# Performance work log

Measured on AMD Instinct MI355X. Metric: run time of the kernel, lower is better.

Reference implementation:

```python
import jax, jax.numpy as jnp
import numpy as np

K = 9          # 3x3 deformable kernel positions
EPS = 1e-5     # BatchNorm eps


def conv3x3(x, w, stride=1):
    # x: [B,C,H,W], w: [O,I,3,3], padding=1
    return jax.lax.conv_general_dilated(
        x, w, (stride, stride), ((1, 1), (1, 1)),
        dimension_numbers=('NCHW', 'OIHW', 'NCHW'))


def _bilinear_sample(img, py, px):
    # img: [C,H,W]; py,px: [K,Ho,Wo] float sample coords (zero outside).
    H, W = img.shape[1], img.shape[2]
    y0 = jnp.floor(py)
    x0 = jnp.floor(px)

    def corner(yc, xc):
        w = (1.0 - jnp.abs(py - yc)) * (1.0 - jnp.abs(px - xc))
        valid = (yc >= 0) & (yc <= H - 1) & (xc >= 0) & (xc <= W - 1)
        yi = jnp.clip(yc, 0, H - 1).astype(jnp.int32)
        xi = jnp.clip(xc, 0, W - 1).astype(jnp.int32)
        v = img[:, yi, xi]                      # [C,K,Ho,Wo]
        return v * (w * valid)[None]

    return (corner(y0, x0) + corner(y0, x0 + 1) +
            corner(y0 + 1, x0) + corner(y0 + 1, x0 + 1))


def deform_conv2d(x, offset, mask, w, stride=1, pad=1):
    # x: [B,Cin,H,W]; offset: [B,2K,Ho,Wo] (y,x interleaved per tap);
    # mask: [B,K,Ho,Wo]; w: [Cout,Cin,3,3]. torchvision DCNv2 semantics.
    B, Cin = x.shape[0], x.shape[1]
    Ho, Wo = offset.shape[2], offset.shape[3]
    Cout = w.shape[0]
    kh, kw = jnp.meshgrid(jnp.arange(3), jnp.arange(3), indexing='ij')
    kh = kh.reshape(K).astype(x.dtype)
    kw = kw.reshape(K).astype(x.dtype)
    base_y = (jnp.arange(Ho) * stride - pad).astype(x.dtype)
    base_x = (jnp.arange(Wo) * stride - pad).astype(x.dtype)
    off = offset.reshape(B, K, 2, Ho, Wo)
    py = base_y[None, None, :, None] + kh[None, :, None, None] + off[:, :, 0]
    px = base_x[None, None, None, :] + kw[None, :, None, None] + off[:, :, 1]
    g = jax.vmap(_bilinear_sample)(x, py, px)     # [B,Cin,K,Ho,Wo]
    g = g * mask[:, None]
    return jnp.einsum('bikhw,oik->bohw', g, w.reshape(Cout, Cin, K))


def batchnorm(x, gamma, beta, mean, var):
    # eval-mode BN over channel dim of [B,C,H,W]
    inv = jax.lax.rsqrt(var + EPS) * gamma
    return x * inv[None, :, None, None] + (beta - mean * inv)[None, :, None, None]


def setup_inputs() -> dict:
    key = jax.random.key(0)
    ks = jax.random.split(key, 20)
    B, Cin, H, W = 16, 64, 64, 64
    C1, C2, NC = 128, 128, 1000
    inp = {
        'x': jax.random.normal(ks[0], (B, Cin, H, W), jnp.float32),
        'conv1_w': jax.random.normal(ks[1], (C1, Cin, 3, 3), jnp.float32) * 0.05,
        'off1_w': jax.random.normal(ks[2], (2 * K, Cin, 3, 3), jnp.float32) * 0.02,
        'mod1_w': jax.random.normal(ks[3], (K, Cin, 3, 3), jnp.float32) * 0.05,
        'bn1_g': jax.random.uniform(ks[4], (C1,), jnp.float32, 0.5, 1.5),
        'bn1_b': jax.random.normal(ks[5], (C1,), jnp.float32) * 0.1,
        'bn1_m': jax.random.normal(ks[6], (C1,), jnp.float32) * 0.1,
        'bn1_v': jax.random.uniform(ks[7], (C1,), jnp.float32, 0.5, 1.5),
        'conv2_w': jax.random.normal(ks[8], (C2, C1, 3, 3), jnp.float32) * 0.05,
        'off2_w': jax.random.normal(ks[9], (2 * K, C1, 3, 3), jnp.float32) * 0.02,
        'mod2_w': jax.random.normal(ks[10], (K, C1, 3, 3), jnp.float32) * 0.05,
        'bn2_g': jax.random.uniform(ks[11], (C2,), jnp.float32, 0.5, 1.5),
        'bn2_b': jax.random.normal(ks[12], (C2,), jnp.float32) * 0.1,
        'bn2_m': jax.random.normal(ks[13], (C2,), jnp.float32) * 0.1,
        'bn2_v': jax.random.uniform(ks[14], (C2,), jnp.float32, 0.5, 1.5),
        'fc_w': jax.random.normal(ks[15], (NC, C2), jnp.float32) * 0.05,
        'fc_b': jnp.zeros((NC,), jnp.float32),
    }
    return inp


def reference(x, conv1_w, off1_w, mod1_w, bn1_g, bn1_b, bn1_m, bn1_v,
              conv2_w, off2_w, mod2_w, bn2_g, bn2_b, bn2_m, bn2_v,
              fc_w, fc_b):
    stride = 1
    # stage 1: deformable conv (offset + sigmoid modulation) + BN + ReLU
    off = conv3x3(x, off1_w, stride)
    mask = jax.nn.sigmoid(conv3x3(x, mod1_w, stride))
    out = deform_conv2d(x, off, mask, conv1_w, stride=stride, pad=1)
    out = jax.nn.relu(batchnorm(out, bn1_g, bn1_b, bn1_m, bn1_v))
    # stage 2: deformable conv + BN (no ReLU before GAP, as in source)
    off = conv3x3(out, off2_w, stride)
    mask = jax.nn.sigmoid(conv3x3(out, mod2_w, stride))
    out = deform_conv2d(out, off, mask, conv2_w, stride=stride, pad=1)
    out = batchnorm(out, bn2_g, bn2_b, bn2_m, bn2_v)
    # global average pool + fc
    out = out.mean(axis=(2, 3))                 # [B, C2]
    return out @ fc_w.T + fc_b
```

## Files before the change

kernel.cpp:

```cpp
#include <hip/hip_runtime.h>

#define TPB 256
typedef unsigned short us;
typedef __attribute__((ext_vector_type(8))) _Float16 f16x8;
typedef __attribute__((ext_vector_type(2))) _Float16 f16x2;
typedef __attribute__((ext_vector_type(4))) float f32x4;

__device__ inline us f2h(float f){ union{ _Float16 h; us u; } x; x.h = (_Float16)f; return x.u; }
__device__ inline f16x2 u2h2(unsigned u){ union{ unsigned v; f16x2 h; } x; x.v = u; return x.h; }
#define MFMA16(a,b,c) __builtin_amdgcn_mfma_f32_16x16x32_f16((a),(b),(c),0,0,0)
#define PERM_LO 0x01000504u
#define PERM_HI 0x03020706u
__device__ inline int swz(int row, int q){ return q ^ ((row ^ (row >> 2)) & 3); }

__global__ __launch_bounds__(256) void k_transpose_x(const float* __restrict__ x,
                                                     us* __restrict__ xT){
  __shared__ float tile[64][65];
  const int y = blockIdx.x, b = blockIdx.y;
  for (int i = threadIdx.x; i < 4096; i += TPB){
    const int c = i >> 6, xx = i & 63;
    tile[c][xx] = x[b*262144 + c*4096 + y*64 + xx];
  }
  __syncthreads();
  for (int i = threadIdx.x; i < 4096; i += TPB){
    const int xx = i >> 6, c = i & 63;
    xT[(size_t)(b*4096 + y*64 + xx)*64 + c] = f2h(tile[c][xx]);
  }
}

__global__ __launch_bounds__(256) void k_prep(
    const float* __restrict__ cw1, const float* __restrict__ ow1, const float* __restrict__ mw1,
    const float* __restrict__ cw2, const float* __restrict__ ow2, const float* __restrict__ mw2,
    us* __restrict__ d1, us* __restrict__ d2, us* __restrict__ a1, us* __restrict__ a2){
  const int e = blockIdx.x*TPB + threadIdx.x;
  if (e < 73728){
    int k = e/8192, r = e%8192, kb = r/4096, r2 = r%4096;
    int n0 = r2>>9, q = r2&511, l = q>>3, j = q&7;
    int co = n0*16 + (l&15), c = kb*32 + (l>>4)*8 + j;
    d1[e] = f2h(cw1[(co*64 + c)*9 + k]);
  }
  if (e < 147456){
    int k = e/16384, r = e%16384, kb = r/4096, r2 = r%4096;
    int n0 = r2>>9, q = r2&511, l = q>>3, j = q&7;
    int co = n0*16 + (l&15), c = kb*32 + (l>>4)*8 + j;
    d2[e] = f2h(cw2[(co*128 + c)*9 + k]);
  }
  if (e < 18432){
    int k = e/2048, r = e%2048, kb = r/1024, r2 = r%1024;
    int n0 = r2>>9, q = r2&511, l = q>>3, j = q&7;
    int co = n0*16 + (l&15), c = kb*32 + (l>>4)*8 + j;
    float w = (co < 18) ? ow1[(co*64 + c)*9 + k] : (co < 27 ? mw1[((co-18)*64 + c)*9 + k] : 0.f);
    a1[e] = f2h(w);
  }
  if (e < 36864){
    int k = e/4096, r = e%4096, kb = r/1024, r2 = r%1024;
    int n0 = r2>>9, q = r2&511, l = q>>3, j = q&7;
    int co = n0*16 + (l&15), c = kb*32 + (l>>4)*8 + j;
    float w = (co < 18) ? ow2[(co*128 + c)*9 + k] : (co < 27 ? mw2[((co-18)*128 + c)*9 + k] : 0.f);
    a2[e] = f2h(w);
  }
}

template<int CIN, int STAGE>
__global__ __launch_bounds__(256, 4) void k_fused(
    const us* __restrict__ inT,
    const us* __restrict__ wb_aux, const us* __restrict__ wb_def,
    const float* __restrict__ bn_g, const float* __restrict__ bn_b,
    const float* __restrict__ bn_m, const float* __restrict__ bn_v,
    us* __restrict__ outT, float* __restrict__ partial){
  constexpr int KB   = CIN/32;
  constexpr int NC   = 9*KB;
  constexpr int WE_A = 2*KB*512;
  constexpr int WE_D = 8*KB*512;

  __shared__ __align__(16) us pool[6336];
  __shared__ uint2 otab[576];
  __shared__ uint2 wtab[576];
  __shared__ float extra[256];

  const int id  = blockIdx.x;
  const int nid = (id & 7)*128 + (id >> 3);
  const int b = nid >> 6, ho = nid & 63;
  const int tid = threadIdx.x;
  const us* __restrict__ inb = inT + (size_t)b*4096*CIN;

  if (STAGE == 1 && tid < 128){
    float inv = rsqrtf(bn_v[tid] + 1e-5f)*bn_g[tid];
    extra[tid] = inv; extra[128 + tid] = bn_b[tid] - bn_m[tid]*inv;
  }

  const int lane = tid & 63, lr = lane & 15, lg = lane >> 4;
  const int wv = tid >> 6;

  f32x4 aacc[2];
  aacc[0] = (f32x4){0.f,0.f,0.f,0.f}; aacc[1] = (f32x4){0.f,0.f,0.f,0.f};
  for (int kb = 0; kb < KB; ++kb){
    if (kb) __syncthreads();
    for (int s = tid; s < 792; s += 256){
      const int slot = s >> 2, cq = s & 3;
      const int r = slot/66, p = slot - r*66;
      const int y = ho - 1 + r, x = p - 1;
      uint4 q = make_uint4(0u,0u,0u,0u);
      if (y >= 0 && y < 64 && x >= 0 && x < 64)
        q = *(const uint4*)(inb + (size_t)(y*64 + x)*CIN + kb*32 + cq*8);
      *(uint4*)(pool + slot*32 + swz(slot, cq)*8) = q;
    }
    __syncthreads();
    #pragma unroll
    for (int k = 0; k < 9; ++k){
      const int kh = k/3, kw = k - kh*3;
      const int slot = kh*66 + wv*16 + lr + kw;
      f16x8 a = *(const f16x8*)(pool + slot*32 + swz(slot, lg)*8);
      #pragma unroll
      for (int n = 0; n < 2; ++n){
        f16x8 bf = *(const f16x8*)(wb_aux + (size_t)k*WE_A + (size_t)(kb*2 + n)*512 + lane*8);
        aacc[n] = MFMA16(a, bf, aacc[n]);
      }
    }
  }
  __syncthreads();

  float* am = (float*)pool;
  #pragma unroll
  for (int n = 0; n < 2; ++n){
    const int co = n*16 + lr;
    if (co < 27){
      #pragma unroll
      for (int i = 0; i < 4; ++i) am[co*66 + wv*16 + lg*4 + i] = aacc[n][i];
    }
  }
  __syncthreads();

  for (int it = 0; it < 3; ++it){
    const int sid = it*256 + tid;
    if (sid < 576){
      const int k = sid >> 6, px = sid & 63;
      const int kh = k/3, kw = k - kh*3;
      float oy = am[(2*k)*66 + px];
      float ox = am[(2*k+1)*66 + px];
      float mv = 1.f/(1.f + expf(-am[(18+k)*66 + px]));
      float py  = (float)(ho - 1 + kh) + oy;
      float pxx = (float)(px - 1 + kw) + ox;
      float fyf = floorf(py), fxf = floorf(pxx);
      int y0 = (int)fyf, x0 = (int)fxf;
      float dy = py - fyf, dx = pxx - fxf;
      bool vy0 = (y0 >= 0) && (y0 < 64), vy1 = (y0 >= -1) && (y0 < 63);
      bool vx0 = (x0 >= 0) && (x0 < 64), vx1 = (x0 >= -1) && (x0 < 63);
      int y0c = min(max(y0,0),63), y1c = min(max(y0+1,0),63);
      int x0c = min(max(x0,0),63), x1c = min(max(x0+1,0),63);
      otab[sid] = make_uint2((unsigned)(y0c*64 + x0c) | ((unsigned)(y0c*64 + x1c) << 16),
                             (unsigned)(y1c*64 + x0c) | ((unsigned)(y1c*64 + x1c) << 16));
      float w00 = (1.f-dy)*(1.f-dx)*mv*((vy0 && vx0) ? 1.f : 0.f);
      float w01 = (1.f-dy)*dx     *mv*((vy0 && vx1) ? 1.f : 0.f);
      float w10 = dy*(1.f-dx)     *mv*((vy1 && vx0) ? 1.f : 0.f);
      float w11 = dy*dx           *mv*((vy1 && vx1) ? 1.f : 0.f);
      wtab[sid] = make_uint2((unsigned)f2h(w00) | ((unsigned)f2h(w01) << 16),
                             (unsigned)f2h(w10) | ((unsigned)f2h(w11) << 16));
    }
  }
  __syncthreads();

  f32x4 acc[4][2];
  #pragma unroll
  for (int m = 0; m < 4; ++m){ acc[m][0] = (f32x4){0.f,0.f,0.f,0.f}; acc[m][1] = (f32x4){0.f,0.f,0.f,0.f}; }

  auto stage_def = [&](int i, us* dst){
    const int k = i/KB, kb = i - (i/KB)*KB;
    const int px = tid >> 2, cq = tid & 3;
    const uint2 o = otab[k*64 + px];
    const uint2 wp = wtab[k*64 + px];
    const f16x2 wAB = u2h2(wp.x), wCD = u2h2(wp.y);
    const int c0 = kb*32 + cq*8;
    const uint4 A = *(const uint4*)(inb + (size_t)(o.x & 0xffffu)*CIN + c0);
    const uint4 B = *(const uint4*)(inb + (size_t)(o.x >> 16)    *CIN + c0);
    const uint4 C = *(const uint4*)(inb + (size_t)(o.y & 0xffffu)*CIN + c0);
    const uint4 D = *(const uint4*)(inb + (size_t)(o.y >> 16)    *CIN + c0);
    const unsigned* Au = (const unsigned*)&A;
    const unsigned* Bu = (const unsigned*)&B;
    const unsigned* Cu = (const unsigned*)&C;
    const unsigned* Du = (const unsigned*)&D;
    uint4 r;
    unsigned* ru = (unsigned*)&r;
    #pragma unroll
    for (int jj = 0; jj < 4; ++jj){
      float vL = __builtin_amdgcn_fdot2(wAB, u2h2(__builtin_amdgcn_perm(Au[jj], Bu[jj], PERM_LO)), 0.f, false);
      vL = __builtin_amdgcn_fdot2(wCD, u2h2(__builtin_amdgcn_perm(Cu[jj], Du[jj], PERM_LO)), vL, false);
      float vH = __builtin_amdgcn_fdot2(wAB, u2h2(__builtin_amdgcn_perm(Au[jj], Bu[jj], PERM_HI)), 0.f, false);
      vH = __builtin_amdgcn_fdot2(wCD, u2h2(__builtin_amdgcn_perm(Cu[jj], Du[jj], PERM_HI)), vH, false);
      ru[jj] = (unsigned)f2h(vL) | ((unsigned)f2h(vH) << 16);
    }
    *(uint4*)(dst + px*32 + swz(px, cq)*8) = r;
  };
  auto mfma_def = [&](int i, const us* src){
    const int k = i/KB, kb = i - (i/KB)*KB;
    f16x8 a[4];
    #pragma unroll
    for (int mt = 0; mt < 4; ++mt){
      const int row = mt*16 + lr;
      a[mt] = *(const f16x8*)(src + row*32 + swz(row, lg)*8);
    }
    #pragma unroll
    for (int nt = 0; nt < 2; ++nt){
      f16x8 bf = *(const f16x8*)(wb_def + (size_t)k*WE_D + (size_t)(kb*8 + wv*2 + nt)*512 + lane*8);
      #pragma unroll
      for (int mt = 0; mt < 4; ++mt)
        acc[mt][nt] = MFMA16(a[mt], bf, acc[mt][nt]);
    }
  };

  us* g0 = pool;
  us* g1 = pool + 2048;
  stage_def(0, g0);
  __syncthreads();
  for (int i = 0; i < NC; ++i){
    us* cur = (i & 1) ? g1 : g0;
    us* nxt = (i & 1) ? g0 : g1;
    if (i + 1 < NC) stage_def(i+1, nxt);
    mfma_def(i, cur);
    __syncthreads();
  }

  if (STAGE == 1){
    const size_t rowbase = (size_t)(b*4096 + ho*64)*128;
    #pragma unroll
    for (int mt = 0; mt < 4; ++mt){
      const int pxl = mt*16 + lg*4;
      #pragma unroll
      for (int nt = 0; nt < 2; ++nt){
        const int co = (wv*2 + nt)*16 + lr;
        const float inv = extra[co], bia = extra[128 + co];
        #pragma unroll
        for (int i = 0; i < 4; ++i){
          float v = acc[mt][nt][i]*inv + bia;
          outT[rowbase + (size_t)(pxl + i)*128 + co] = f2h(fmaxf(v, 0.f));
        }
      }
    }
  } else {
    #pragma unroll
    for (int nt = 0; nt < 2; ++nt){
      float s = 0.f;
      #pragma unroll
      for (int mt = 0; mt < 4; ++mt)
        s += acc[mt][nt][0] + acc[mt][nt][1] + acc[mt][nt][2] + acc[mt][nt][3];
      s += __shfl_xor(s, 16);
      s += __shfl_xor(s, 32);
      if (lane < 16) extra[(wv*2 + nt)*16 + lane] = s;
    }
    __syncthreads();
    if (tid < 128) partial[(size_t)(b*64 + ho)*128 + tid] = extra[tid];
  }
}

__global__ __launch_bounds__(256) void k_pool(
    const float* __restrict__ partial,
    const float* __restrict__ g2, const float* __restrict__ b2,
    const float* __restrict__ m2, const float* __restrict__ v2,
    float* __restrict__ pooled){
  const int t = blockIdx.x*TPB + threadIdx.x;
  if (t >= 2048) return;
  const int b = t >> 7, c = t & 127;
  float s = 0.f;
  for (int h = 0; h < 64; ++h) s += partial[(b*64 + h)*128 + c];
  const float inv = rsqrtf(v2[c] + 1e-5f)*g2[c];
  pooled[t] = s*(1.f/4096.f)*inv + (b2[c] - m2[c]*inv);
}

__global__ __launch_bounds__(256) void k_fc(
    const float* __restrict__ pooled, const float* __restrict__ fcw,
    const float* __restrict__ fcb, float* __restrict__ outp){
  const int t = blockIdx.x*TPB + threadIdx.x;
  if (t >= 16000) return;
  const int b = t/1000, n = t - b*1000;
  const float* p = pooled + b*128;
  const float* w = fcw + n*128;
  float s = fcb[n];
  #pragma unroll
  for (int c = 0; c < 128; c += 4){
    const float4 pv = *(const float4*)(p + c);
    const float4 wv = *(const float4*)(w + c);
    s = fmaf(pv.x, wv.x, s); s = fmaf(pv.y, wv.y, s);
    s = fmaf(pv.z, wv.z, s); s = fmaf(pv.w, wv.w, s);
  }
  outp[t] = s;
}

extern "C" void kernel_launch(void* const* d_in, const int* in_sizes, int n_in,
                              void* d_out, int out_size, void* d_ws, size_t ws_size,
                              hipStream_t stream){
  const float* x      = (const float*)d_in[0];
  const float* conv1w = (const float*)d_in[1];
  const float* off1w  = (const float*)d_in[2];
  const float* mod1w  = (const float*)d_in[3];
  const float* bn1g   = (const float*)d_in[4];
  const float* bn1b   = (const float*)d_in[5];
  const float* bn1m   = (const float*)d_in[6];
  const float* bn1v   = (const float*)d_in[7];
  const float* conv2w = (const float*)d_in[8];
  const float* off2w  = (const float*)d_in[9];
  const float* mod2w  = (const float*)d_in[10];
  const float* bn2g   = (const float*)d_in[11];
  const float* bn2b   = (const float*)d_in[12];
  const float* bn2m   = (const float*)d_in[13];
  const float* bn2v   = (const float*)d_in[14];
  const float* fcw    = (const float*)d_in[15];
  const float* fcb    = (const float*)d_in[16];

  char* w = (char*)d_ws;
  us*    xT      = (us*)(w);
  us*    out1T   = (us*)(w + 8388608);
  float* partial = (float*)(w + 25165824);
  float* pooled  = (float*)(w + 25690112);
  us*    wb_d1   = (us*)(w + 25698304);
  us*    wb_d2   = (us*)(w + 25845760);
  us*    wb_a1   = (us*)(w + 26140672);
  us*    wb_a2   = (us*)(w + 26177536);

  k_transpose_x<<<dim3(64,16), TPB, 0, stream>>>(x, xT);
  k_prep<<<576, TPB, 0, stream>>>(conv1w, off1w, mod1w, conv2w, off2w, mod2w,
                                  wb_d1, wb_d2, wb_a1, wb_a2);

  k_fused<64,1><<<1024, TPB, 0, stream>>>(
      xT, wb_a1, wb_d1, bn1g, bn1b, bn1m, bn1v, out1T, nullptr);
  k_fused<128,2><<<1024, TPB, 0, stream>>>(
      out1T, wb_a2, wb_d2, nullptr, nullptr, nullptr, nullptr, nullptr, partial);

  k_pool<<<8, TPB, 0, stream>>>(partial, bn2g, bn2b, bn2m, bn2v, pooled);
  k_fc<<<63, TPB, 0, stream>>>(pooled, fcw, fcb, (float*)d_out);
}
```

Measured before the change: 112.5 us.

## Use 512-thread blocks with 64-channel K-chunks and packed f16 bilinear blend

Doubles the fused deformable-conv block to 8 waves. Each wave now owns one 16-channel output tile instead of two, and each pipeline step stages 64 input channels instead of 32, which halves the number of barrier-separated steps. The bilinear blend switches from perm+fdot2 to packed f16 vector multiply-adds, and the LDS swizzle becomes a simple XOR over 8 chunks. In exchange, shared memory per block roughly doubles and per-wave MFMA work halves. Interpolation now accumulates in f16 rather than f32, which may reduce accuracy.

```diff
diff --git a/kernel.cpp b/kernel.cpp
--- a/kernel.cpp
+++ b/kernel.cpp
@@ -9,9 +9,6 @@
 __device__ inline us f2h(float f){ union{ _Float16 h; us u; } x; x.h = (_Float16)f; return x.u; }
 __device__ inline f16x2 u2h2(unsigned u){ union{ unsigned v; f16x2 h; } x; x.v = u; return x.h; }
 #define MFMA16(a,b,c) __builtin_amdgcn_mfma_f32_16x16x32_f16((a),(b),(c),0,0,0)
-#define PERM_LO 0x01000504u
-#define PERM_HI 0x03020706u
-__device__ inline int swz(int row, int q){ return q ^ ((row ^ (row >> 2)) & 3); }
 
 __global__ __launch_bounds__(256) void k_transpose_x(const float* __restrict__ x,
                                                      us* __restrict__ xT){
@@ -62,18 +59,18 @@
 }
 
 template<int CIN, int STAGE>
-__global__ __launch_bounds__(256, 4) void k_fused(
+__global__ __launch_bounds__(512, 6) void k_fused(
     const us* __restrict__ inT,
     const us* __restrict__ wb_aux, const us* __restrict__ wb_def,
     const float* __restrict__ bn_g, const float* __restrict__ bn_b,
     const float* __restrict__ bn_m, const float* __restrict__ bn_v,
     us* __restrict__ outT, float* __restrict__ partial){
-  constexpr int KB   = CIN/32;
-  constexpr int NC   = 9*KB;
-  constexpr int WE_A = 2*KB*512;
-  constexpr int WE_D = 8*KB*512;
-
-  __shared__ __align__(16) us pool[6336];
+  constexpr int KB2  = CIN/64;
+  constexpr int NC   = 9*KB2;
+  constexpr int WE_A = 2*(CIN/32)*512;
+  constexpr int WE_D = 8*(CIN/32)*512;
+
+  __shared__ __align__(16) us pool[12672];
   __shared__ uint2 otab[576];
   __shared__ uint2 wtab[576];
   __shared__ float extra[256];
@@ -92,124 +89,115 @@
   const int lane = tid & 63, lr = lane & 15, lg = lane >> 4;
   const int wv = tid >> 6;
 
-  f32x4 aacc[2];
-  aacc[0] = (f32x4){0.f,0.f,0.f,0.f}; aacc[1] = (f32x4){0.f,0.f,0.f,0.f};
-  for (int kb = 0; kb < KB; ++kb){
-    if (kb) __syncthreads();
-    for (int s = tid; s < 792; s += 256){
-      const int slot = s >> 2, cq = s & 3;
+  const int mh = wv & 3, nh = wv >> 2;
+  f32x4 aacc = (f32x4){0.f,0.f,0.f,0.f};
+  for (int kb2 = 0; kb2 < KB2; ++kb2){
+    if (kb2) __syncthreads();
+    for (int s = tid; s < 1584; s += 512){
+      const int slot = s >> 3, cq = s & 7;
       const int r = slot/66, p = slot - r*66;
       const int y = ho - 1 + r, x = p - 1;
       uint4 q = make_uint4(0u,0u,0u,0u);
       if (y >= 0 && y < 64 && x >= 0 && x < 64)
-        q = *(const uint4*)(inb + (size_t)(y*64 + x)*CIN + kb*32 + cq*8);
-      *(uint4*)(pool + slot*32 + swz(slot, cq)*8) = q;
+        q = *(const uint4*)(inb + (size_t)(y*64 + x)*CIN + kb2*64 + cq*8);
+      *(uint4*)(pool + slot*64 + ((cq ^ (slot & 7))*8)) = q;
     }
     __syncthreads();
     #pragma unroll
     for (int k = 0; k < 9; ++k){
       const int kh = k/3, kw = k - kh*3;
-      const int slot = kh*66 + wv*16 + lr + kw;
-      f16x8 a = *(const f16x8*)(pool + slot*32 + swz(slot, lg)*8);
+      const int slot = kh*66 + mh*16 + lr + kw;
       #pragma unroll
-      for (int n = 0; n < 2; ++n){
-        f16x8 bf = *(const f16x8*)(wb_aux + (size_t)k*WE_A + (size_t)(kb*2 + n)*512 + lane*8);
-        aacc[n] = MFMA16(a, bf, aacc[n]);
+      for (int kbl = 0; kbl < 2; ++kbl){
+        f16x8 a = *(const f16x8*)(pool + slot*64 + (((kbl*4 + lg) ^ (slot & 7))*8));
+        f16x8 bf = *(const f16x8*)(wb_aux + (size_t)k*WE_A + (size_t)((kb2*2 + kbl)*2 + nh)*512 + lane*8);
+        aacc = MFMA16(a, bf, aacc);
       }
     }
   }
   __syncthreads();
 
   float* am = (float*)pool;
-  #pragma unroll
-  for (int n = 0; n < 2; ++n){
-    const int co = n*16 + lr;
+  {
+    const int co = nh*16 + lr;
     if (co < 27){
       #pragma unroll
-      for (int i = 0; i < 4; ++i) am[co*66 + wv*16 + lg*4 + i] = aacc[n][i];
-    }
-  }
-  __syncthreads();
-
-  for (int it = 0; it < 3; ++it){
-    const int sid = it*256 + tid;
-    if (sid < 576){
-      const int k = sid >> 6, px = sid & 63;
-      const int kh = k/3, kw = k - kh*3;
-      float oy = am[(2*k)*66 + px];
-      float ox = am[(2*k+1)*66 + px];
-      float mv = 1.f/(1.f + expf(-am[(18+k)*66 + px]));
-      float py  = (float)(ho - 1 + kh) + oy;
-      float pxx = (float)(px - 1 + kw) + ox;
-      float fyf = floorf(py), fxf = floorf(pxx);
-      int y0 = (int)fyf, x0 = (int)fxf;
-      float dy = py - fyf, dx = pxx - fxf;
-      bool vy0 = (y0 >= 0) && (y0 < 64), vy1 = (y0 >= -1) && (y0 < 63);
-      bool vx0 = (x0 >= 0) && (x0 < 64), vx1 = (x0 >= -1) && (x0 < 63);
-      int y0c = min(max(y0,0),63), y1c = min(max(y0+1,0),63);
-      int x0c = min(max(x0,0),63), x1c = min(max(x0+1,0),63);
-      otab[sid] = make_uint2((unsigned)(y0c*64 + x0c) | ((unsigned)(y0c*64 + x1c) << 16),
-                             (unsigned)(y1c*64 + x0c) | ((unsigned)(y1c*64 + x1c) << 16));
-      float w00 = (1.f-dy)*(1.f-dx)*mv*((vy0 && vx0) ? 1.f : 0.f);
-      float w01 = (1.f-dy)*dx     *mv*((vy0 && vx1) ? 1.f : 0.f);
-      float w10 = dy*(1.f-dx)     *mv*((vy1 && vx0) ? 1.f : 0.f);
-      float w11 = dy*dx           *mv*((vy1 && vx1) ? 1.f : 0.f);
-      wtab[sid] = make_uint2((unsigned)f2h(w00) | ((unsigned)f2h(w01) << 16),
-                             (unsigned)f2h(w10) | ((unsigned)f2h(w11) << 16));
-    }
-  }
-  __syncthreads();
-
-  f32x4 acc[4][2];
+      for (int i = 0; i < 4; ++i) am[co*66 + mh*16 + lg*4 + i] = aacc[i];
+    }
+  }
+  __syncthreads();
+
+  for (int sid = tid; sid < 576; sid += 512){
+    const int k = sid >> 6, px = sid & 63;
+    const int kh = k/3, kw = k - kh*3;
+    float oy = am[(2*k)*66 + px];
+    float ox = am[(2*k+1)*66 + px];
+    float mv = 1.f/(1.f + expf(-am[(18+k)*66 + px]));
+    float py  = (float)(ho - 1 + kh) + oy;
+    float pxx = (float)(px - 1 + kw) + ox;
+    float fyf = floorf(py), fxf = floorf(pxx);
+    int y0 = (int)fyf, x0 = (int)fxf;
+    float dy = py - fyf, dx = pxx - fxf;
+    bool vy0 = (y0 >= 0) && (y0 < 64), vy1 = (y0 >= -1) && (y0 < 63);
+    bool vx0 = (x0 >= 0) && (x0 < 64), vx1 = (x0 >= -1) && (x0 < 63);
+    int y0c = min(max(y0,0),63), y1c = min(max(y0+1,0),63);
+    int x0c = min(max(x0,0),63), x1c = min(max(x0+1,0),63);
+    otab[sid] = make_uint2((unsigned)(y0c*64 + x0c) | ((unsigned)(y0c*64 + x1c) << 16),
+                           (unsigned)(y1c*64 + x0c) | ((unsigned)(y1c*64 + x1c) << 16));
+    float w00 = (1.f-dy)*(1.f-dx)*mv*((vy0 && vx0) ? 1.f : 0.f);
+    float w01 = (1.f-dy)*dx     *mv*((vy0 && vx1) ? 1.f : 0.f);
+    float w10 = dy*(1.f-dx)     *mv*((vy1 && vx0) ? 1.f : 0.f);
+    float w11 = dy*dx           *mv*((vy1 && vx1) ? 1.f : 0.f);
+    wtab[sid] = make_uint2((unsigned)f2h(w00) | ((unsigned)f2h(w01) << 16),
+                           (unsigned)f2h(w10) | ((unsigned)f2h(w11) << 16));
+  }
+  __syncthreads();
+
+  f32x4 acc[4];
   #pragma unroll
-  for (int m = 0; m < 4; ++m){ acc[m][0] = (f32x4){0.f,0.f,0.f,0.f}; acc[m][1] = (f32x4){0.f,0.f,0.f,0.f}; }
+  for (int m = 0; m < 4; ++m) acc[m] = (f32x4){0.f,0.f,0.f,0.f};
 
   auto stage_def = [&](int i, us* dst){
-    const int k = i/KB, kb = i - (i/KB)*KB;
-    const int px = tid >> 2, cq = tid & 3;
+    const int k = i/KB2, kb2 = i - (i/KB2)*KB2;
+    const int px = tid >> 3, cq = tid & 7;
     const uint2 o = otab[k*64 + px];
     const uint2 wp = wtab[k*64 + px];
     const f16x2 wAB = u2h2(wp.x), wCD = u2h2(wp.y);
-    const int c0 = kb*32 + cq*8;
-    const uint4 A = *(const uint4*)(inb + (size_t)(o.x & 0xffffu)*CIN + c0);
-    const uint4 B = *(const uint4*)(inb + (size_t)(o.x >> 16)    *CIN + c0);
-    const uint4 C = *(const uint4*)(inb + (size_t)(o.y & 0xffffu)*CIN + c0);
-    const uint4 D = *(const uint4*)(inb + (size_t)(o.y >> 16)    *CIN + c0);
-    const unsigned* Au = (const unsigned*)&A;
-    const unsigned* Bu = (const unsigned*)&B;
-    const unsigned* Cu = (const unsigned*)&C;
-    const unsigned* Du = (const unsigned*)&D;
-    uint4 r;
-    unsigned* ru = (unsigned*)&r;
-    #pragma unroll
-    for (int jj = 0; jj < 4; ++jj){
-      float vL = __builtin_amdgcn_fdot2(wAB, u2h2(__builtin_amdgcn_perm(Au[jj], Bu[jj], PERM_LO)), 0.f, false);
-      vL = __builtin_amdgcn_fdot2(wCD, u2h2(__builtin_amdgcn_perm(Cu[jj], Du[jj], PERM_LO)), vL, false);
-      float vH = __builtin_amdgcn_fdot2(wAB, u2h2(__builtin_amdgcn_perm(Au[jj], Bu[jj], PERM_HI)), 0.f, false);
-      vH = __builtin_amdgcn_fdot2(wCD, u2h2(__builtin_amdgcn_perm(Cu[jj], Du[jj], PERM_HI)), vH, false);
-      ru[jj] = (unsigned)f2h(vL) | ((unsigned)f2h(vH) << 16);
-    }
-    *(uint4*)(dst + px*32 + swz(px, cq)*8) = r;
+    const _Float16 wA = wAB[0], wB = wAB[1], wC = wCD[0], wD = wCD[1];
+    const f16x8 va = (f16x8){wA,wA,wA,wA,wA,wA,wA,wA};
+    const f16x8 vb = (f16x8){wB,wB,wB,wB,wB,wB,wB,wB};
+    const f16x8 vc = (f16x8){wC,wC,wC,wC,wC,wC,wC,wC};
+    const f16x8 vd = (f16x8){wD,wD,wD,wD,wD,wD,wD,wD};
+    const int c0 = kb2*64 + cq*8;
+    f16x8 r;
+    {
+      const f16x8 A = *(const f16x8*)(inb + (size_t)(o.x & 0xffffu)*CIN + c0);
+      const f16x8 B = *(const f16x8*)(inb + (size_t)(o.x >> 16)    *CIN + c0);
+      r = A*va + B*vb;
+    }
+    {
+      const f16x8 C = *(const f16x8*)(inb + (size_t)(o.y & 0xffffu)*CIN + c0);
+      const f16x8 D = *(const f16x8*)(inb + (size_t)(o.y >> 16)    *CIN + c0);
+      r = r + C*vc + D*vd;
+    }
+    *(f16x8*)(dst + px*64 + ((cq ^ (px & 7))*8)) = r;
   };
   auto mfma_def = [&](int i, const us* src){
-    const int k = i/KB, kb = i - (i/KB)*KB;
-    f16x8 a[4];
+    const int k = i/KB2, kb2 = i - (i/KB2)*KB2;
     #pragma unroll
-    for (int mt = 0; mt < 4; ++mt){
-      const int row = mt*16 + lr;
-      a[mt] = *(const f16x8*)(src + row*32 + swz(row, lg)*8);
-    }
-    #pragma unroll
-    for (int nt = 0; nt < 2; ++nt){
-      f16x8 bf = *(const f16x8*)(wb_def + (size_t)k*WE_D + (size_t)(kb*8 + wv*2 + nt)*512 + lane*8);
+    for (int kbl = 0; kbl < 2; ++kbl){
+      f16x8 bf = *(const f16x8*)(wb_def + (size_t)k*WE_D + (size_t)((kb2*2 + kbl)*8 + wv)*512 + lane*8);
       #pragma unroll
-      for (int mt = 0; mt < 4; ++mt)
-        acc[mt][nt] = MFMA16(a[mt], bf, acc[mt][nt]);
+      for (int mt = 0; mt < 4; ++mt){
+        const int row = mt*16 + lr;
+        f16x8 a = *(const f16x8*)(src + row*64 + (((kbl*4 + lg) ^ (row & 7))*8));
+        acc[mt] = MFMA16(a, bf, acc[mt]);
+      }
     }
   };
 
   us* g0 = pool;
-  us* g1 = pool + 2048;
+  us* g1 = pool + 4096;
   stage_def(0, g0);
   __syncthreads();
   for (int i = 0; i < NC; ++i){
@@ -222,31 +210,25 @@
 
   if (STAGE == 1){
     const size_t rowbase = (size_t)(b*4096 + ho*64)*128;
+    const int co = wv*16 + lr;
+    const float inv = extra[co], bia = extra[128 + co];
     #pragma unroll
     for (int mt = 0; mt < 4; ++mt){
       const int pxl = mt*16 + lg*4;
       #pragma unroll
-      for (int nt = 0; nt < 2; ++nt){
-        const int co = (wv*2 + nt)*16 + lr;
-        const float inv = extra[co], bia = extra[128 + co];
-        #pragma unroll
-        for (int i = 0; i < 4; ++i){
-          float v = acc[mt][nt][i]*inv + bia;
-          outT[rowbase + (size_t)(pxl + i)*128 + co] = f2h(fmaxf(v, 0.f));
-        }
+      for (int i = 0; i < 4; ++i){
+        float v = acc[mt][i]*inv + bia;
+        outT[rowbase + (size_t)(pxl + i)*128 + co] = f2h(fmaxf(v, 0.f));
       }
     }
   } else {
+    float s = 0.f;
     #pragma unroll
-    for (int nt = 0; nt < 2; ++nt){
-      float s = 0.f;
-      #pragma unroll
-      for (int mt = 0; mt < 4; ++mt)
-        s += acc[mt][nt][0] + acc[mt][nt][1] + acc[mt][nt][2] + acc[mt][nt][3];
-      s += __shfl_xor(s, 16);
-      s += __shfl_xor(s, 32);
-      if (lane < 16) extra[(wv*2 + nt)*16 + lane] = s;
-    }
+    for (int mt = 0; mt < 4; ++mt)
+      s += acc[mt][0] + acc[mt][1] + acc[mt][2] + acc[mt][3];
+    s += __shfl_xor(s, 16);
+    s += __shfl_xor(s, 32);
+    if (lane < 16) extra[wv*16 + lane] = s;
     __syncthreads();
     if (tid < 128) partial[(size_t)(b*64 + ho)*128 + tid] = extra[tid];
   }
@@ -320,9 +302,9 @@
   k_prep<<<576, TPB, 0, stream>>>(conv1w, off1w, mod1w, conv2w, off2w, mod2w,
                                   wb_d1, wb_d2, wb_a1, wb_a2);
 
-  k_fused<64,1><<<1024, TPB, 0, stream>>>(
+  k_fused<64,1><<<1024, 512, 0, stream>>>(
       xT, wb_a1, wb_d1, bn1g, bn1b, bn1m, bn1v, out1T, nullptr);
-  k_fused<128,2><<<1024, TPB, 0, stream>>>(
+  k_fused<128,2><<<1024, 512, 0, stream>>>(
       out1T, wb_a2, wb_d2, nullptr, nullptr, nullptr, nullptr, nullptr, partial);
 
   k_pool<<<8, TPB, 0, stream>>>(partial, bn2g, bn2b, bn2m, bn2v, pooled);
```

Result: slower. 119.8 us (+6.5%).
